# Optimization experiments

Hardware: AMD Instinct MI355X
Metric: run time of the kernel (lower is better)

Reference implementation:

```python
import jax, jax.numpy as jnp
import numpy as np

V, H, L, NH, MAXS = 32000, 1024, 6, 16, 2048
HD = H // NH
FF = 4 * H
EPS = 1e-5


def _ln(x, s, b):
    m = jnp.mean(x, axis=-1, keepdims=True)
    v = jnp.mean(jnp.square(x - m), axis=-1, keepdims=True)
    return (x - m) * jax.lax.rsqrt(v + EPS) * s + b


def setup_inputs() -> dict:
    key = jax.random.key(0)
    ks = jax.random.split(key, 12)
    s = 0.02
    inp = {
        "input_ids": jax.random.randint(ks[0], (2, 1024), 0, V, dtype=jnp.int64),
        "token_emb": jax.random.normal(ks[1], (V, H), jnp.float32) * s,
        "pos_emb": jax.random.normal(ks[2], (MAXS, H), jnp.float32) * s,
        "ln1_s": jnp.ones((L, H), jnp.float32),
        "ln1_b": jnp.zeros((L, H), jnp.float32),
        "qkv_w": jax.random.normal(ks[3], (L, H, 3 * H), jnp.float32) * s,
        "qkv_b": jnp.zeros((L, 3 * H), jnp.float32),
        "out_w": jax.random.normal(ks[4], (L, H, H), jnp.float32) * s,
        "out_b": jnp.zeros((L, H), jnp.float32),
        "ln2_s": jnp.ones((L, H), jnp.float32),
        "ln2_b": jnp.zeros((L, H), jnp.float32),
        "w1": jax.random.normal(ks[5], (L, H, FF), jnp.float32) * s,
        "b1": jnp.zeros((L, FF), jnp.float32),
        "w2": jax.random.normal(ks[6], (L, FF, H), jnp.float32) * s,
        "b2": jnp.zeros((L, H), jnp.float32),
        "lnf_s": jnp.ones((H,), jnp.float32),
        "lnf_b": jnp.zeros((H,), jnp.float32),
        "lm_w": jax.random.normal(ks[7], (H, V), jnp.float32) * s,
    }
    return inp


def reference(input_ids, token_emb, pos_emb, ln1_s, ln1_b, qkv_w, qkv_b,
              out_w, out_b, ln2_s, ln2_b, w1, b1, w2, b2, lnf_s, lnf_b, lm_w):
    B, S = input_ids.shape
    x = token_emb[input_ids] + pos_emb[:S][None]  # [B,S,H]; dropout = identity (eval)
    for i in range(L):
        # --- attention block ---
        h = _ln(x, ln1_s[i], ln1_b[i])
        qkv = h @ qkv_w[i] + qkv_b[i]                      # [B,S,3H]
        q, k, v = jnp.split(qkv, 3, axis=-1)
        q = q.reshape(B, S, NH, HD)
        k = k.reshape(B, S, NH, HD)
        v = v.reshape(B, S, NH, HD)
        scores = jnp.einsum('bqhd,bkhd->bhqk', q, k) / jnp.sqrt(jnp.float32(HD))
        attn = jax.nn.softmax(scores, axis=-1)             # non-causal, as in source
        o = jnp.einsum('bhqk,bkhd->bqhd', attn, v).reshape(B, S, H)
        x = x + o @ out_w[i] + out_b[i]
        # --- mlp block ---
        h = _ln(x, ln2_s[i], ln2_b[i])
        h = jax.nn.gelu(h @ w1[i] + b1[i], approximate=False)
        x = x + h @ w2[i] + b2[i]
    x = _ln(x, lnf_s, lnf_b)
    logits = x @ lm_w                                      # [B,S,V]
    return logits
```

## Files before the change

kernel.cpp:

```cpp
#include <hip/hip_runtime.h>
#include <hip/hip_bf16.h>
#include <cstdint>
#include <cstddef>

typedef __bf16 bf16;
typedef __attribute__((ext_vector_type(8))) __bf16 bf16x8;
typedef __attribute__((ext_vector_type(4))) __bf16 bf16x4;
typedef __attribute__((ext_vector_type(4))) float f32x4;

__device__ __forceinline__ f32x4 mfma16(bf16x8 a, bf16x8 b, f32x4 c) {
    return __builtin_amdgcn_mfma_f32_16x16x32_bf16(a, b, c, 0, 0, 0);
}

__device__ __forceinline__ void async_copy16(const void* g, void* l) {
    __builtin_amdgcn_global_load_lds((const __attribute__((address_space(1))) void*)g,
                                     (__attribute__((address_space(3))) void*)l,
                                     16, 0, 0);
}

template<int Ncnt> __device__ __forceinline__ void waitv();
template<> __device__ __forceinline__ void waitv<0>() { asm volatile("s_waitcnt vmcnt(0)" ::: "memory"); }
template<> __device__ __forceinline__ void waitv<2>() { asm volatile("s_waitcnt vmcnt(2)" ::: "memory"); }
template<> __device__ __forceinline__ void waitv<3>() { asm volatile("s_waitcnt vmcnt(3)" ::: "memory"); }
template<> __device__ __forceinline__ void waitv<4>() { asm volatile("s_waitcnt vmcnt(4)" ::: "memory"); }

__device__ __forceinline__ void wait_g(int n) {
    if (n == 2) waitv<2>();
    else if (n == 3) waitv<3>();
    else waitv<4>();
}

__device__ __forceinline__ void ln_vec(f32x4 v, const float* __restrict__ sc,
                                       const float* __restrict__ bi, bf16* __restrict__ out,
                                       int row, int t, float* red)
{
    float s = v[0] + v[1] + v[2] + v[3];
    float q = v[0]*v[0] + v[1]*v[1] + v[2]*v[2] + v[3]*v[3];
    #pragma unroll
    for (int o = 1; o < 64; o <<= 1) { s += __shfl_xor(s, o); q += __shfl_xor(q, o); }
    const int wv = t >> 6, lane = t & 63;
    if (lane == 0) { red[wv] = s; red[4 + wv] = q; }
    __syncthreads();
    s = red[0] + red[1] + red[2] + red[3];
    q = red[4] + red[5] + red[6] + red[7];
    const float mean = s * (1.f / 1024.f);
    const float var  = q * (1.f / 1024.f) - mean * mean;
    const float rstd = rsqrtf(var + 1e-5f);
    const f32x4 scv = ((const f32x4*)sc)[t];
    const f32x4 biv = ((const f32x4*)bi)[t];
    bf16x4 o4;
    #pragma unroll
    for (int j = 0; j < 4; j++) o4[j] = (bf16)((v[j] - mean) * rstd * scv[j] + biv[j]);
    *(bf16x4*)(out + (size_t)row * 1024 + t * 4) = o4;
}

__device__ __forceinline__ void ln_body(const float* __restrict__ x, const float* __restrict__ sc,
                                        const float* __restrict__ bi, bf16* __restrict__ out,
                                        int row, int t, float* red)
{
    const f32x4 v = ((const f32x4*)(x + (size_t)row * 1024))[t];
    ln_vec(v, sc, bi, out, row, t, red);
}

__device__ __forceinline__ void wcvt_body(const float* __restrict__ W, bf16* __restrict__ BT,
                                          int K, int N, int bid, int tidx, float (*tile)[65])
{
    const int nx = N >> 6;
    const int n0 = (bid % nx) << 6, k0 = (bid / nx) << 6;
    const int tx = tidx & 15, ty = tidx >> 4;
    #pragma unroll
    for (int r = 0; r < 4; r++) {
        const f32x4 v = *(const f32x4*)&W[(size_t)(k0 + ty + r*16) * N + n0 + tx*4];
        tile[ty + r*16][tx*4 + 0] = v[0];
        tile[ty + r*16][tx*4 + 1] = v[1];
        tile[ty + r*16][tx*4 + 2] = v[2];
        tile[ty + r*16][tx*4 + 3] = v[3];
    }
    __syncthreads();
    #pragma unroll
    for (int r = 0; r < 4; r++) {
        const int n = ty + r*16;
        bf16x4 o;
        #pragma unroll
        for (int j = 0; j < 4; j++) o[j] = (bf16)tile[tx*4 + j][n];
        *(bf16x4*)&BT[(size_t)(n0 + n) * K + k0 + tx*4] = o;
    }
}

__global__ __launch_bounds__(256)
void front_kernel(const int* __restrict__ ids, const float* __restrict__ te,
                  const float* __restrict__ pe, float* __restrict__ x,
                  const float* __restrict__ sc, const float* __restrict__ bi,
                  bf16* __restrict__ out,
                  const float* __restrict__ qkvw0, bf16* __restrict__ wTq)
{
    __shared__ float tile[64][65];
    __shared__ float red[8];
    const int bid = blockIdx.x, t = threadIdx.x;
    if (bid < 2048) {
        const int s = bid & 1023;
        const int id = ids[bid];
        const f32x4 a = ((const f32x4*)(te + (size_t)id * 1024))[t];
        const f32x4 b = ((const f32x4*)(pe + (size_t)s * 1024))[t];
        const f32x4 v = a + b;
        ((f32x4*)(x + (size_t)bid * 1024))[t] = v;
        ln_vec(v, sc, bi, out, bid, t, red);
    } else {
        wcvt_body(qkvw0, wTq, 1024, 3072, bid - 2048, t, tile);
    }
}

__global__ __launch_bounds__(256)
void ln_kernel(const float* __restrict__ x, const float* __restrict__ sc,
               const float* __restrict__ bi, bf16* __restrict__ out)
{
    __shared__ float red[8];
    ln_body(x, sc, bi, out, blockIdx.x, threadIdx.x, red);
}

__global__ __launch_bounds__(256)
void attn_wcvt_kernel(const bf16* __restrict__ qkv, const bf16* __restrict__ vT,
                      bf16* __restrict__ attno,
                      const float* __restrict__ qkvw_n, bf16* __restrict__ wTq_n, int nbq,
                      const float* __restrict__ w1, bf16* __restrict__ wT1,
                      const float* __restrict__ w2, bf16* __restrict__ wT2,
                      const float* __restrict__ outw, bf16* __restrict__ wTo,
                      const float* __restrict__ lmw, bf16* __restrict__ wTlm, int lm_lo)
{
    __shared__ __align__(16) char smem[49664];
    const int bid = blockIdx.x, tid = threadIdx.x;

    if (bid >= 512) {
        float (*tile)[65] = (float(*)[65])smem;
        int wb = bid - 512;
        if (wb < nbq) { wcvt_body(qkvw_n, wTq_n, 1024, 3072, wb, tid, tile); return; }
        wb -= nbq;
        if (wb < 1024) { wcvt_body(w1, wT1, 1024, 4096, wb, tid, tile); return; }
        wb -= 1024;
        if (wb < 1024) { wcvt_body(w2, wT2, 4096, 1024, wb, tid, tile); return; }
        wb -= 1024;
        if (wb < 256)  { wcvt_body(outw, wTo, 1024, 1024, wb, tid, tile); return; }
        wb -= 256;
        wcvt_body(lmw, wTlm, 1024, 32000, lm_lo + wb, tid, tile);
        return;
    }

    bf16* Ksh = (bf16*)smem;
    bf16* Vt  = (bf16*)(smem + 16384);
    bf16* Plds = (bf16*)(smem + 32768);
#define PLDS(w_, r_, c_) Plds[(((w_) << 4) + (r_)) * 132 + (c_)]

    const int b = (bid & 31) >> 4, h = bid & 15;
    const int qb = bid >> 5;
    const int lane = tid & 63, wave = tid >> 6;
    const bf16* base = qkv + (size_t)b * 1024 * 3072;
    const bf16* vbase = vT + (size_t)(b*16 + h) * 64 * 1024;
    const int qrow0 = qb * 64 + wave * 16;
    const int l15 = lane & 15;

    bf16x8 aQ[2];
    {
        const int qr = qrow0 + l15;
        const bf16* qp = base + (size_t)qr * 3072 + h * 64 + ((lane >> 4) << 3);
        aQ[0] = *(const bf16x8*)qp;
        aQ[1] = *(const bf16x8*)(qp + 32);
    }
    float m_i[4] = {-1e30f, -1e30f, -1e30f, -1e30f};
    float l_i[4] = {0.f, 0.f, 0.f, 0.f};
    f32x4 acc[4];
    #pragma unroll
    for (int nb = 0; nb < 4; nb++) acc[nb] = f32x4{0.f, 0.f, 0.f, 0.f};

    const int swzA = (((lane >> 4)     ^ (lane & 7)) << 3);
    const int swzB = (((4 + (lane >> 4)) ^ (lane & 7)) << 3);

    for (int ck = 0; ck < 8; ck++) {
        __syncthreads();
        #pragma unroll
        for (int p = 0; p < 4; p++) {
            const int c = p * 256 + tid;
            const int rw = c >> 3;
            const int kc = (c & 7) ^ (rw & 7);
            async_copy16(base + (size_t)(ck*128 + rw) * 3072 + 1024 + h*64 + kc*8, &Ksh[c * 8]);
        }
        #pragma unroll
        for (int p = 0; p < 4; p++) {
            const int c = p * 256 + tid;
            const int rw = c >> 4;
            const int kc = (c & 15) ^ (rw & 7);
            async_copy16(vbase + (size_t)rw * 1024 + ck*128 + kc*8, &Vt[c * 8]);
        }
        waitv<4>();
        __builtin_amdgcn_sched_barrier(0);
        __builtin_amdgcn_s_barrier();

        f32x4 sc[8];
        #pragma unroll
        for (int kk = 0; kk < 4; kk++) {
            const int kr0 = (kk*32 + l15) * 64;
            const int kr1 = kr0 + 16*64;
            f32x4 z{0.f, 0.f, 0.f, 0.f};
            z = mfma16(aQ[0], *(const bf16x8*)&Ksh[kr0 + swzA], z);
            z = mfma16(aQ[1], *(const bf16x8*)&Ksh[kr0 + swzB], z);
            sc[2*kk] = z;
            f32x4 z2{0.f, 0.f, 0.f, 0.f};
            z2 = mfma16(aQ[0], *(const bf16x8*)&Ksh[kr1 + swzA], z2);
            z2 = mfma16(aQ[1], *(const bf16x8*)&Ksh[kr1 + swzB], z2);
            sc[2*kk+1] = z2;
        }

        float c[4];
        #pragma unroll
        for (int i = 0; i < 4; i++) {
            float t = sc[0][i];
            #pragma unroll
            for (int e = 1; e < 8; e++) t = fmaxf(t, sc[e][i]);
            #pragma unroll
            for (int o = 1; o < 16; o <<= 1) t = fmaxf(t, __shfl_xor(t, o));
            t *= 0.125f;
            const float mnew = fmaxf(m_i[i], t);
            c[i] = __expf(m_i[i] - mnew);
            float p[8];
            float rs = 0.f;
            #pragma unroll
            for (int e = 0; e < 8; e++) {
                p[e] = __expf(fmaf(sc[e][i], 0.125f, -mnew));
                rs += p[e];
            }
            #pragma unroll
            for (int o = 1; o < 16; o <<= 1) rs += __shfl_xor(rs, o);
            l_i[i] = l_i[i] * c[i] + rs;
            m_i[i] = mnew;
            const int pr = ((lane >> 4) << 2) + i;
            #pragma unroll
            for (int e = 0; e < 8; e++)
                PLDS(wave, pr, (e >> 1) * 32 + (e & 1) * 16 + l15) = (bf16)p[e];
        }

        waitv<0>();
        __builtin_amdgcn_sched_barrier(0);
        __builtin_amdgcn_s_barrier();

        #pragma unroll
        for (int nb = 0; nb < 4; nb++) {
            f32x4 a = acc[nb];
            a[0] *= c[0]; a[1] *= c[1]; a[2] *= c[2]; a[3] *= c[3];
            acc[nb] = a;
        }
        #pragma unroll
        for (int kk = 0; kk < 4; kk++) {
            const bf16x8 aP = *(const bf16x8*)&PLDS(wave, l15, kk*32 + ((lane >> 4) << 3));
            #pragma unroll
            for (int nb = 0; nb < 4; nb++) {
                const int r = nb*16 + l15;
                const int chk = (kk*4 + (lane >> 4)) ^ (r & 7);
                const bf16x8 bV = *(const bf16x8*)&Vt[r*128 + chk*8];
                acc[nb] = mfma16(aP, bV, acc[nb]);
            }
        }
    }
    #pragma unroll
    for (int nb = 0; nb < 4; nb++) {
        #pragma unroll
        for (int i = 0; i < 4; i++) {
            const int row = qrow0 + ((lane >> 4) << 2) + i;
            const float o = acc[nb][i] / l_i[i];
            attno[(size_t)(b*1024 + row) * 1024 + h*64 + nb*16 + l15] = (bf16)o;
        }
    }
#undef PLDS
}

template<int BM, int BN, int EPI, int KSPLIT>
__global__ __launch_bounds__(512, 2)
void gemm256_kernel(const bf16* __restrict__ A, const bf16* __restrict__ BT,
                    const float* __restrict__ bias, float* __restrict__ resid,
                    bf16* __restrict__ outb, float* __restrict__ outf,
                    bf16* __restrict__ vt, int N, int K)
{
    constexpr int MT = 2048 / BM;
    constexpr int FM = BM / 32;
    constexpr int FN = BN / 64;
    constexpr int HM = FM / 2;
    constexpr int ACH = BM * 4;
    constexpr int BCH = BN * 4;
    constexpr int LA = (ACH + 511) >> 9;
    constexpr int LB = (BCH + 511) >> 9;
    constexpr int ASUB = BM * 32;
    constexpr int BSUB = BN * 32;
    extern __shared__ __align__(16) char smem_raw[];
    bf16* smem = (bf16*)smem_raw;

    const int nwg = gridDim.x;
    const int q = nwg >> 3, rr = nwg & 7;
    const int xcd = blockIdx.x & 7, ix = blockIdx.x >> 3;
    const int nid = (xcd < rr ? xcd * (q + 1) : rr * (q + 1) + (xcd - rr) * q) + ix;
    const int tiles = nwg / KSPLIT;
    const int ks = nid / tiles;
    const int tile = nid % tiles;
    const int bm = tile % MT, bn = tile / MT;

    const int tid = threadIdx.x, lane = tid & 63, wave = tid >> 6;
    const int wr = wave >> 2, wc = wave & 3;

    const int myB = ((BCH & 511) == 0) ? (BCH >> 9)
                    : ((tid < (BCH & 511)) ? (BCH >> 9) + 1 : (BCH >> 9));
    const int wcount = LA + myB;

    f32x4 acc[FM][FN];
    #pragma unroll
    for (int m = 0; m < FM; m++)
        #pragma unroll
        for (int n = 0; n < FN; n++) acc[m][n] = f32x4{0.f, 0.f, 0.f, 0.f};

    const bf16* Abase = A  + (size_t)bm * BM * K;
    const bf16* Bbase = BT + (size_t)bn * BN * K;
    const int Ts = (K >> 6) / KSPLIT;
    const int t0 = ks * Ts;

    const int l15 = lane & 15;
    const int swz = (((lane >> 4) ^ ((l15 >> 1) & 3)) << 3);
    const int arow0 = wr * (BM / 2) + l15;
    const int brow0 = wc * (BN / 4) + l15;

#define ABASE_(p_, ks_) (((p_)*2 + (ks_)) * ASUB)
#define BBASE_(p_, ks_) (4*ASUB + ((p_)*2 + (ks_)) * BSUB)
#define STAGE_A(p_, kt_, ks_) { _Pragma("unroll") for (int i = 0; i < LA; i++) { \
    const int c = tid + i * 512; \
    if ((ACH & 511) == 0 || c < ACH) { \
      const int rw = c >> 2; \
      const int kc = (c & 3) ^ ((rw >> 1) & 3); \
      async_copy16(Abase + (size_t)rw * K + (kt_)*64 + (ks_)*32 + kc*8, \
                   &smem[ABASE_(p_, ks_) + c*8]); } } }
#define STAGE_B(p_, kt_, ks_) { _Pragma("unroll") for (int i = 0; i < LB; i++) { \
    const int c = tid + i * 512; \
    if ((BCH & 511) == 0 || c < BCH) { \
      const int rw = c >> 2; \
      const int kc = (c & 3) ^ ((rw >> 1) & 3); \
      async_copy16(Bbase + (size_t)rw * K + (kt_)*64 + (ks_)*32 + kc*8, \
                   &smem[BBASE_(p_, ks_) + c*8]); } } }
#define LOAD_B(p_, ks_) { _Pragma("unroll") for (int n = 0; n < FN; n++) \
    bfv[n] = *(const bf16x8*)&smem[BBASE_(p_, ks_) + (brow0 + n*16)*32 + swz]; }
#define LOAD_A(p_, ks_, mg) { _Pragma("unroll") for (int m = 0; m < HM; m++) \
    af[m] = *(const bf16x8*)&smem[ABASE_(p_, ks_) + (arow0 + ((mg)*HM + m)*16)*32 + swz]; }
#define QUAD(mg) { __builtin_amdgcn_s_setprio(1); \
    _Pragma("unroll") for (int m = 0; m < HM; m++) \
      _Pragma("unroll") for (int n = 0; n < FN; n++) \
        acc[(mg)*HM + m][n] = mfma16(af[m], bfv[n], acc[(mg)*HM + m][n]); \
    __builtin_amdgcn_s_setprio(0); }

    STAGE_A(0, t0, 0); STAGE_B(0, t0, 0); STAGE_A(0, t0, 1); STAGE_B(0, t0, 1);
    wait_g(wcount);
    __builtin_amdgcn_s_barrier();

    for (int tl = 0; tl < Ts; tl++) {
        const int b = tl & 1;
        const int kt1 = t0 + tl + 1;
        const bool more = (tl + 1) < Ts;
        bf16x8 af[HM], bfv[FN];
        LOAD_B(b, 0); LOAD_A(b, 0, 0);
        if (more) STAGE_A(b ^ 1, kt1, 0);
        __builtin_amdgcn_s_barrier();
        QUAD(0);
        __builtin_amdgcn_s_barrier();
        LOAD_A(b, 0, 1);
        if (more) STAGE_B(b ^ 1, kt1, 0);
        __builtin_amdgcn_s_barrier();
        QUAD(1);
        if (more) wait_g(wcount); else waitv<0>();
        __builtin_amdgcn_s_barrier();
        LOAD_B(b, 1); LOAD_A(b, 1, 0);
        if (more) STAGE_A(b ^ 1, kt1, 1);
        __builtin_amdgcn_s_barrier();
        QUAD(0);
        __builtin_amdgcn_s_barrier();
        LOAD_A(b, 1, 1);
        if (more) STAGE_B(b ^ 1, kt1, 1);
        __builtin_amdgcn_s_barrier();
        QUAD(1);
        if (more) wait_g(wcount);
        __builtin_amdgcn_s_barrier();
    }

    const int er = bm * BM + wr * (BM / 2) + ((lane >> 4) << 2);
    const int ec = bn * BN + wc * (BN / 4) + l15;
    #pragma unroll
    for (int n = 0; n < FN; n++) {
        const int col = ec + n * 16;
        const float bv = (EPI == 3) ? 0.f : ((KSPLIT > 1 && ks != 0) ? 0.f : bias[col]);
        #pragma unroll
        for (int m = 0; m < FM; m++) {
            const int row0 = er + m * 16;
            if constexpr (EPI == 4) {
                if (col < 2048) {
                    #pragma unroll
                    for (int i = 0; i < 4; i++)
                        outb[(size_t)(row0 + i) * N + col] = (bf16)(acc[m][n][i] + bv);
                } else {
                    bf16x4 o4;
                    #pragma unroll
                    for (int i = 0; i < 4; i++) o4[i] = (bf16)(acc[m][n][i] + bv);
                    const int b_ = row0 >> 10, tok = row0 & 1023;
                    *(bf16x4*)&vt[((size_t)(b_ * 1024 + (col - 2048))) * 1024 + tok] = o4;
                }
            } else {
                #pragma unroll
                for (int i = 0; i < 4; i++) {
                    const float v = acc[m][n][i] + bv;
                    const size_t off = (size_t)(row0 + i) * N + col;
                    if constexpr (EPI == 0) outb[off] = (bf16)v;
                    else if constexpr (EPI == 1) {
                        if constexpr (KSPLIT > 1) atomicAdd(&resid[off], v);
                        else resid[off] += v;
                    }
                    else if constexpr (EPI == 2) {
                        outb[off] = (bf16)(0.5f * v * (1.f + erff(v * 0.70710678118f)));
                    } else {
                        outf[off] = v;
                    }
                }
            }
        }
    }
#undef ABASE_
#undef BBASE_
#undef STAGE_A
#undef STAGE_B
#undef LOAD_A
#undef LOAD_B
#undef QUAD
}

extern "C" void kernel_launch(void* const* d_in, const int* in_sizes, int n_in,
                              void* d_out, int out_size, void* d_ws, size_t ws_size,
                              hipStream_t stream)
{
    const int*   ids     = (const int*)  d_in[0];
    const float* tok_emb = (const float*)d_in[1];
    const float* pos_emb = (const float*)d_in[2];
    const float* ln1_s   = (const float*)d_in[3];
    const float* ln1_b   = (const float*)d_in[4];
    const float* qkv_w   = (const float*)d_in[5];
    const float* qkv_b   = (const float*)d_in[6];
    const float* out_w   = (const float*)d_in[7];
    const float* out_b   = (const float*)d_in[8];
    const float* ln2_s   = (const float*)d_in[9];
    const float* ln2_b   = (const float*)d_in[10];
    const float* w1      = (const float*)d_in[11];
    const float* b1      = (const float*)d_in[12];
    const float* w2      = (const float*)d_in[13];
    const float* b2      = (const float*)d_in[14];
    const float* lnf_s   = (const float*)d_in[15];
    const float* lnf_b   = (const float*)d_in[16];
    const float* lm_w    = (const float*)d_in[17];

    char* ws = (char*)d_ws;
    float* x    = (float*)ws;  ws += (size_t)2048 * 1024 * 4;
    bf16*  h    = (bf16*)ws;   ws += (size_t)2048 * 1024 * 2;
    bf16*  qkvb = (bf16*)ws;   ws += (size_t)2048 * 3072 * 2;
    bf16*  attno= (bf16*)ws;   ws += (size_t)2048 * 1024 * 2;
    bf16*  vT   = (bf16*)ws;   ws += (size_t)32 * 64 * 1024 * 2;
    bf16*  ff   = (bf16*)ws;   ws += (size_t)2048 * 4096 * 2;
    bf16*  wTq2 = (bf16*)ws;   ws += (size_t)2 * 3072 * 1024 * 2;
    bf16*  wTo_all = (bf16*)ws; ws += (size_t)6 * 1024 * 1024 * 2;
    bf16*  wT1  = (bf16*)ws;   ws += (size_t)4096 * 1024 * 2;
    bf16*  wT2  = (bf16*)ws;   ws += (size_t)1024 * 4096 * 2;
    bf16*  wTlm = (bf16*)ws;   ws += (size_t)32000 * 1024 * 2;

    for (int l = 0; l < 6; l++) {
        bf16* wTq_cur = wTq2 + (size_t)(l & 1) * 3072 * 1024;
        bf16* wTq_nxt = wTq2 + (size_t)((l + 1) & 1) * 3072 * 1024;
        if (l == 0) {
            front_kernel<<<2816, 256, 0, stream>>>(
                ids, tok_emb, pos_emb, x, ln1_s, ln1_b, h, qkv_w, wTq_cur);
        } else {
            ln_kernel<<<2048, 256, 0, stream>>>(x, ln1_s + l*1024, ln1_b + l*1024, h);
        }
        gemm256_kernel<128,192,4,1><<<256, 512, 81920, stream>>>(
            h, wTq_cur, qkv_b + l*3072, nullptr, qkvb, nullptr, vT, 3072, 1024);
        const int nbq = (l < 5) ? 768 : 0;
        const int lm_lo = (8000 * l) / 6;
        const int lm_cnt = (8000 * (l + 1)) / 6 - lm_lo;
        attn_wcvt_kernel<<<512 + nbq + 1024 + 1024 + 256 + lm_cnt, 256, 0, stream>>>(
            qkvb, vT, attno,
            (l < 5) ? qkv_w + (size_t)(l+1)*1024*3072 : nullptr, wTq_nxt, nbq,
            w1 + (size_t)l*1024*4096, wT1,
            w2 + (size_t)l*4096*1024, wT2,
            out_w + (size_t)l*1024*1024, wTo_all + (size_t)l*1024*1024,
            lm_w, wTlm, lm_lo);
        gemm256_kernel<128,256,1,4><<<256, 512, 98304, stream>>>(
            attno, wTo_all + (size_t)l*1024*1024, out_b + l*1024, x, nullptr, nullptr, nullptr, 1024, 1024);
        ln_kernel<<<2048, 256, 0, stream>>>(x, ln2_s + l*1024, ln2_b + l*1024, h);
        gemm256_kernel<128,256,2,1><<<256, 512, 98304, stream>>>(
            h, wT1, b1 + l*4096, nullptr, ff, nullptr, nullptr, 4096, 1024);
        gemm256_kernel<128,256,1,4><<<256, 512, 98304, stream>>>(
            ff, wT2, b2 + l*1024, x, nullptr, nullptr, nullptr, 1024, 4096);
    }
    ln_kernel<<<2048, 256, 0, stream>>>(x, lnf_s, lnf_b, h);
    gemm256_kernel<256,256,3,1><<<8*125, 512, 131072, stream>>>(
        h, wTlm, nullptr, nullptr, nullptr, (float*)d_out, nullptr, 32000, 1024);
}
```

Before: 1.226 ms.

## Fuse next-layer LayerNorm into split-K MLP down-projection GEMM via per-row-block counters

Adds a dedicated split-K MLP2 GEMM that atomically accumulates into the residual. Each workgroup bumps a per-row-block counter and spins until all 16 tiles of that row block are done, then computes LayerNorm for 8 rows and writes the bf16 input for the next layer (or the final LN). This removes six standalone LN launches and one full pass over x. The cost is a spin-wait that needs all 256 workgroups resident at once, and the counters are cleared by the preceding ln2 kernel.

```diff
diff --git a/kernel.cpp b/kernel.cpp
--- a/kernel.cpp
+++ b/kernel.cpp
@@ -112,9 +112,11 @@
 
 __global__ __launch_bounds__(256)
 void ln_kernel(const float* __restrict__ x, const float* __restrict__ sc,
-               const float* __restrict__ bi, bf16* __restrict__ out)
+               const float* __restrict__ bi, bf16* __restrict__ out,
+               int* __restrict__ cnt_zero)
 {
     __shared__ float red[8];
+    if (blockIdx.x == 0 && threadIdx.x < 16) cnt_zero[threadIdx.x] = 0;
     ln_body(x, sc, bi, out, blockIdx.x, threadIdx.x, red);
 }
 
@@ -431,6 +433,165 @@
 #undef QUAD
 }
 
+__global__ __launch_bounds__(512, 2)
+void gemm_mlp2ln_kernel(const bf16* __restrict__ A, const bf16* __restrict__ BT,
+                        const float* __restrict__ bias, float* __restrict__ resid,
+                        int* __restrict__ cnt,
+                        const float* __restrict__ lnS, const float* __restrict__ lnB,
+                        bf16* __restrict__ hout, int N, int K)
+{
+    constexpr int BM = 128, BN = 256, KSPLIT = 4;
+    constexpr int MT = 16, FM = 4, FN = 4, HM = 2, LA = 1, LB = 2;
+    constexpr int ASUB = BM * 32, BSUB = BN * 32;
+    extern __shared__ __align__(16) char smem_raw[];
+    bf16* smem = (bf16*)smem_raw;
+
+    const int nwg = gridDim.x;
+    const int q = nwg >> 3, rr = nwg & 7;
+    const int xcd = blockIdx.x & 7, ix = blockIdx.x >> 3;
+    const int nid = (xcd < rr ? xcd * (q + 1) : rr * (q + 1) + (xcd - rr) * q) + ix;
+    const int tiles = nwg / KSPLIT;
+    const int ks = nid / tiles;
+    const int tile = nid % tiles;
+    const int bm = tile % MT, bn = tile / MT;
+
+    const int tid = threadIdx.x, lane = tid & 63, wave = tid >> 6;
+    const int wr = wave >> 2, wc = wave & 3;
+
+    f32x4 acc[FM][FN];
+    #pragma unroll
+    for (int m = 0; m < FM; m++)
+        #pragma unroll
+        for (int n = 0; n < FN; n++) acc[m][n] = f32x4{0.f, 0.f, 0.f, 0.f};
+
+    const bf16* Abase = A  + (size_t)bm * BM * K;
+    const bf16* Bbase = BT + (size_t)bn * BN * K;
+    const int Ts = (K >> 6) / KSPLIT;
+    const int t0 = ks * Ts;
+
+    const int l15 = lane & 15;
+    const int swz = (((lane >> 4) ^ ((l15 >> 1) & 3)) << 3);
+    const int arow0 = wr * (BM / 2) + l15;
+    const int brow0 = wc * (BN / 4) + l15;
+
+#define ABASE_(p_, ks_) (((p_)*2 + (ks_)) * ASUB)
+#define BBASE_(p_, ks_) (4*ASUB + ((p_)*2 + (ks_)) * BSUB)
+#define STAGE_A(p_, kt_, ks_) { \
+    const int c = tid; const int rw = c >> 2; \
+    const int kc = (c & 3) ^ ((rw >> 1) & 3); \
+    async_copy16(Abase + (size_t)rw * K + (kt_)*64 + (ks_)*32 + kc*8, \
+                 &smem[ABASE_(p_, ks_) + c*8]); }
+#define STAGE_B(p_, kt_, ks_) { _Pragma("unroll") for (int i = 0; i < LB; i++) { \
+    const int c = tid + i * 512; const int rw = c >> 2; \
+    const int kc = (c & 3) ^ ((rw >> 1) & 3); \
+    async_copy16(Bbase + (size_t)rw * K + (kt_)*64 + (ks_)*32 + kc*8, \
+                 &smem[BBASE_(p_, ks_) + c*8]); } }
+#define LOAD_B(p_, ks_) { _Pragma("unroll") for (int n = 0; n < FN; n++) \
+    bfv[n] = *(const bf16x8*)&smem[BBASE_(p_, ks_) + (brow0 + n*16)*32 + swz]; }
+#define LOAD_A(p_, ks_, mg) { _Pragma("unroll") for (int m = 0; m < HM; m++) \
+    af[m] = *(const bf16x8*)&smem[ABASE_(p_, ks_) + (arow0 + ((mg)*HM + m)*16)*32 + swz]; }
+#define QUAD(mg) { __builtin_amdgcn_s_setprio(1); \
+    _Pragma("unroll") for (int m = 0; m < HM; m++) \
+      _Pragma("unroll") for (int n = 0; n < FN; n++) \
+        acc[(mg)*HM + m][n] = mfma16(af[m], bfv[n], acc[(mg)*HM + m][n]); \
+    __builtin_amdgcn_s_setprio(0); }
+
+    STAGE_A(0, t0, 0); STAGE_B(0, t0, 0); STAGE_A(0, t0, 1); STAGE_B(0, t0, 1);
+    waitv<3>();
+    __builtin_amdgcn_s_barrier();
+
+    for (int tl = 0; tl < Ts; tl++) {
+        const int b = tl & 1;
+        const int kt1 = t0 + tl + 1;
+        const bool more = (tl + 1) < Ts;
+        bf16x8 af[HM], bfv[FN];
+        LOAD_B(b, 0); LOAD_A(b, 0, 0);
+        if (more) STAGE_A(b ^ 1, kt1, 0);
+        __builtin_amdgcn_s_barrier();
+        QUAD(0);
+        __builtin_amdgcn_s_barrier();
+        LOAD_A(b, 0, 1);
+        if (more) STAGE_B(b ^ 1, kt1, 0);
+        __builtin_amdgcn_s_barrier();
+        QUAD(1);
+        if (more) waitv<3>(); else waitv<0>();
+        __builtin_amdgcn_s_barrier();
+        LOAD_B(b, 1); LOAD_A(b, 1, 0);
+        if (more) STAGE_A(b ^ 1, kt1, 1);
+        __builtin_amdgcn_s_barrier();
+        QUAD(0);
+        __builtin_amdgcn_s_barrier();
+        LOAD_A(b, 1, 1);
+        if (more) STAGE_B(b ^ 1, kt1, 1);
+        __builtin_amdgcn_s_barrier();
+        QUAD(1);
+        if (more) waitv<3>();
+        __builtin_amdgcn_s_barrier();
+    }
+
+    const int er = bm * BM + wr * 64 + ((lane >> 4) << 2);
+    const int ec = bn * BN + wc * 64 + l15;
+    #pragma unroll
+    for (int n = 0; n < FN; n++) {
+        const int col = ec + n * 16;
+        const float bv = (ks != 0) ? 0.f : bias[col];
+        #pragma unroll
+        for (int m = 0; m < FM; m++) {
+            #pragma unroll
+            for (int i = 0; i < 4; i++) {
+                const float v = acc[m][n][i] + bv;
+                atomicAdd(&resid[(size_t)(er + m * 16 + i) * N + col], v);
+            }
+        }
+    }
+
+    __threadfence();
+    __syncthreads();
+    if (tid == 0) {
+        atomicAdd(cnt + bm, 1);
+        while (__hip_atomic_load(cnt + bm, __ATOMIC_ACQUIRE, __HIP_MEMORY_SCOPE_AGENT) < 16)
+            __builtin_amdgcn_s_sleep(8);
+    }
+    __syncthreads();
+    __threadfence();
+    {
+        float* red = (float*)smem_raw;
+        const int rank = ks * 4 + bn;
+        const int sub = tid >> 8, tt = tid & 255;
+        const int wv8 = tid >> 6;
+        #pragma unroll
+        for (int it = 0; it < 4; it++) {
+            const int row = bm * 128 + rank * 8 + it * 2 + sub;
+            const f32x4 v = ((const f32x4*)(resid + (size_t)row * 1024))[tt];
+            float s = v[0] + v[1] + v[2] + v[3];
+            float qq = v[0]*v[0] + v[1]*v[1] + v[2]*v[2] + v[3]*v[3];
+            #pragma unroll
+            for (int o = 1; o < 64; o <<= 1) { s += __shfl_xor(s, o); qq += __shfl_xor(qq, o); }
+            if ((tid & 63) == 0) { red[wv8] = s; red[8 + wv8] = qq; }
+            __syncthreads();
+            s  = red[sub*4+0] + red[sub*4+1] + red[sub*4+2] + red[sub*4+3];
+            qq = red[8+sub*4+0] + red[8+sub*4+1] + red[8+sub*4+2] + red[8+sub*4+3];
+            const float mean = s * (1.f / 1024.f);
+            const float var  = qq * (1.f / 1024.f) - mean * mean;
+            const float rstd = rsqrtf(var + 1e-5f);
+            const f32x4 scv = ((const f32x4*)lnS)[tt];
+            const f32x4 biv = ((const f32x4*)lnB)[tt];
+            bf16x4 o4;
+            #pragma unroll
+            for (int j = 0; j < 4; j++) o4[j] = (bf16)((v[j] - mean) * rstd * scv[j] + biv[j]);
+            *(bf16x4*)(hout + (size_t)row * 1024 + tt * 4) = o4;
+            __syncthreads();
+        }
+    }
+#undef ABASE_
+#undef BBASE_
+#undef STAGE_A
+#undef STAGE_B
+#undef LOAD_A
+#undef LOAD_B
+#undef QUAD
+}
+
 extern "C" void kernel_launch(void* const* d_in, const int* in_sizes, int n_in,
                               void* d_out, int out_size, void* d_ws, size_t ws_size,
                               hipStream_t stream)
@@ -466,6 +627,7 @@
     bf16*  wT1  = (bf16*)ws;   ws += (size_t)4096 * 1024 * 2;
     bf16*  wT2  = (bf16*)ws;   ws += (size_t)1024 * 4096 * 2;
     bf16*  wTlm = (bf16*)ws;   ws += (size_t)32000 * 1024 * 2;
+    int*   cnts = (int*)ws;    ws += (size_t)6 * 16 * 4;
 
     for (int l = 0; l < 6; l++) {
         bf16* wTq_cur = wTq2 + (size_t)(l & 1) * 3072 * 1024;
@@ -473,8 +635,6 @@
         if (l == 0) {
             front_kernel<<<2816, 256, 0, stream>>>(
                 ids, tok_emb, pos_emb, x, ln1_s, ln1_b, h, qkv_w, wTq_cur);
-        } else {
-            ln_kernel<<<2048, 256, 0, stream>>>(x, ln1_s + l*1024, ln1_b + l*1024, h);
         }
         gemm256_kernel<128,192,4,1><<<256, 512, 81920, stream>>>(
             h, wTq_cur, qkv_b + l*3072, nullptr, qkvb, nullptr, vT, 3072, 1024);
@@ -490,13 +650,15 @@
             lm_w, wTlm, lm_lo);
         gemm256_kernel<128,256,1,4><<<256, 512, 98304, stream>>>(
             attno, wTo_all + (size_t)l*1024*1024, out_b + l*1024, x, nullptr, nullptr, nullptr, 1024, 1024);
-        ln_kernel<<<2048, 256, 0, stream>>>(x, ln2_s + l*1024, ln2_b + l*1024, h);
+        ln_kernel<<<2048, 256, 0, stream>>>(x, ln2_s + l*1024, ln2_b + l*1024, h, cnts + l*16);
         gemm256_kernel<128,256,2,1><<<256, 512, 98304, stream>>>(
             h, wT1, b1 + l*4096, nullptr, ff, nullptr, nullptr, 4096, 1024);
-        gemm256_kernel<128,256,1,4><<<256, 512, 98304, stream>>>(
-            ff, wT2, b2 + l*1024, x, nullptr, nullptr, nullptr, 1024, 4096);
-    }
-    ln_kernel<<<2048, 256, 0, stream>>>(x, lnf_s, lnf_b, h);
+        gemm_mlp2ln_kernel<<<256, 512, 98304, stream>>>(
+            ff, wT2, b2 + l*1024, x, cnts + l*16,
+            (l < 5) ? ln1_s + (l+1)*1024 : lnf_s,
+            (l < 5) ? ln1_b + (l+1)*1024 : lnf_b,
+            h, 1024, 4096);
+    }
     gemm256_kernel<256,256,3,1><<<8*125, 512, 131072, stream>>>(
         h, wTlm, nullptr, nullptr, nullptr, (float*)d_out, nullptr, 32000, 1024);
 }
```

Measured after the change: 1.690 ms. +37.9%, slower.
